# Performance work log

Measured on AMD Instinct MI355X. Metric: run time of the kernel, lower is better.

The kernel has to match this reference:

```python
import jax, jax.numpy as jnp
import numpy as np

H = 12  # num_attention_heads
D = 64  # size_per_head


def setup_inputs() -> dict:
    key = jax.random.key(0)
    ks = jax.random.split(key, 6)
    B, S, W = 4, 2048, H * D
    x = jax.random.normal(ks[0], (B, S, W), dtype=jnp.float32)
    segment_ids = jax.random.randint(ks[1], (B, S), 0, 2, dtype=jnp.int32)
    std = 0.02
    Wq = jax.random.normal(ks[2], (W, W), dtype=jnp.float32) * std
    Wk = jax.random.normal(ks[3], (W, W), dtype=jnp.float32) * std
    Wv = jax.random.normal(ks[4], (W, W), dtype=jnp.float32) * std
    zeros = jnp.zeros((W,), dtype=jnp.float32)
    return {"x": x, "segment_ids": segment_ids, "Wq": Wq, "bq": zeros,
            "Wk": Wk, "bk": zeros, "Wv": Wv, "bv": zeros}


def reference(x, segment_ids, Wq, bq, Wk, bk, Wv, bv):
    B, S, W = x.shape
    # linear projections (no activation; defaults are None)
    q = (x @ Wq + bq).reshape(B, S, H, D).transpose(0, 2, 1, 3)  # [B,H,S,D]
    k = (x @ Wk + bk).reshape(B, S, H, D).transpose(0, 2, 1, 3)
    v = (x @ Wv + bv).reshape(B, S, H, D).transpose(0, 2, 1, 3)
    scores = jnp.einsum('bhqd,bhkd->bhqk', q, k) / jnp.sqrt(jnp.float32(D))
    # UniLM seq2seq bias: position j visible to i iff cumsum(s)[j] <= cumsum(s)[i]
    idxs = jnp.cumsum(segment_ids.astype(jnp.float32), axis=1)  # [B,S]
    mask = (idxs[:, None, :] <= idxs[:, :, None]).astype(jnp.float32)  # [B,S,S]
    bias = -(1.0 - mask) * 1e12
    scores = scores + bias[:, None, :, :]
    probs = jax.nn.softmax(scores, axis=-1)
    ctx = jnp.einsum('bhqk,bhkd->bhqd', probs, v)  # [B,H,S,D]
    return ctx.transpose(0, 2, 1, 3).reshape(B, S, H * D)
```

## Files before the change

### kernel.cpp

```cpp
#include <hip/hip_runtime.h>
#include <hip/hip_bf16.h>

#define NB 4
#define NS 2048
#define NH 12
#define ND 64
#define NW 768
#define HBUF (NB * NH * NS * ND)
#define QBLK 128
#define QSCALE 0.18033688f

typedef __attribute__((ext_vector_type(8))) short bf16x8;
typedef __attribute__((ext_vector_type(4))) float f32x4;
typedef __attribute__((ext_vector_type(16))) float f32x16;

__device__ inline unsigned short f2bf_bits(float f) {
  __hip_bfloat16 h = __float2bfloat16(f);
  union { __hip_bfloat16 h; unsigned short u; } c; c.h = h; return c.u;
}
__device__ inline void gload16(const void* g, void* l) {
  __builtin_amdgcn_global_load_lds(
      (const __attribute__((address_space(1))) unsigned int*)g,
      (__attribute__((address_space(3))) unsigned int*)l, 16, 0, 0);
}
#define EXP_SC 8388608.0f
#define EXP_BI 1064986882.0f

__global__ __launch_bounds__(256) void prep_kernel(
    const float* __restrict__ x, const int* __restrict__ seg,
    const float* __restrict__ Wq, const float* __restrict__ Wk,
    const float* __restrict__ Wv, __hip_bfloat16* __restrict__ xbf,
    __hip_bfloat16* __restrict__ Wt, int* __restrict__ cum) {
  __shared__ float tile[64][65];
  __shared__ int sums[256];
  const int bid = blockIdx.x;
  const int t = threadIdx.x;

  if (bid < 1024) {
    const int n8 = NB * NS * NW / 8;
    for (int i = bid * 256 + t; i < n8; i += 1024 * 256) {
      const float4 a = ((const float4*)x)[i * 2];
      const float4 b = ((const float4*)x)[i * 2 + 1];
      bf16x8 o;
      o[0] = (short)f2bf_bits(a.x); o[1] = (short)f2bf_bits(a.y);
      o[2] = (short)f2bf_bits(a.z); o[3] = (short)f2bf_bits(a.w);
      o[4] = (short)f2bf_bits(b.x); o[5] = (short)f2bf_bits(b.y);
      o[6] = (short)f2bf_bits(b.z); o[7] = (short)f2bf_bits(b.w);
      *(bf16x8*)((unsigned short*)xbf + (size_t)i * 8) = o;
    }
  } else if (bid < 1456) {
    const int idx = bid - 1024;
    const int m = idx / 144, rem = idx % 144;
    const float* W = (m == 0) ? Wq : ((m == 1) ? Wk : Wv);
    const int rt = (rem / 12) * 64, ct = (rem % 12) * 64;
#pragma unroll
    for (int j = 0; j < 4; ++j) {
      const int r = j * 16 + (t >> 4);
      const int c = (t & 15) * 4;
      const float4 v = *(const float4*)(W + (size_t)(rt + r) * NW + ct + c);
      tile[r][c] = v.x; tile[r][c + 1] = v.y; tile[r][c + 2] = v.z; tile[r][c + 3] = v.w;
    }
    __syncthreads();
#pragma unroll
    for (int j = 0; j < 2; ++j) {
      const int i2 = j * 256 + t;
      const int nn = i2 >> 3, kq = (i2 & 7) * 8;
      bf16x8 o;
#pragma unroll
      for (int e = 0; e < 8; ++e) o[e] = (short)f2bf_bits(tile[kq + e][nn]);
      *(bf16x8*)((unsigned short*)Wt + (size_t)(m * NW + ct + nn) * NW + rt + kq) = o;
    }
  } else {
    const int b = bid - 1456;
    int vals[8];
    int s = 0;
    const int base = b * NS + t * 8;
#pragma unroll
    for (int j = 0; j < 8; ++j) { vals[j] = seg[base + j]; s += vals[j]; }
    sums[t] = s;
    __syncthreads();
    int acc = s;
    for (int off = 1; off < 256; off <<= 1) {
      const int u = (t >= off) ? sums[t - off] : 0;
      __syncthreads();
      acc += u;
      sums[t] = acc;
      __syncthreads();
    }
    int prefix = acc - s;
#pragma unroll
    for (int j = 0; j < 8; ++j) { prefix += vals[j]; cum[base + j] = prefix; }
  }
}

__global__ __launch_bounds__(256) void qkv_gemm_kernel(
    const __hip_bfloat16* __restrict__ A, const __hip_bfloat16* __restrict__ Bt,
    const float* __restrict__ bq, const float* __restrict__ bk,
    const float* __restrict__ bv, __hip_bfloat16* __restrict__ O,
    __hip_bfloat16* __restrict__ Vt) {
  __shared__ __align__(16) char As[128 * 128];
  __shared__ __align__(16) char Bs[128 * 128];
  const int t = threadIdx.x, lane = t & 63, w = t >> 6;
  const int l15 = lane & 15, lhi = lane >> 4;
  const int wg = (blockIdx.x & 7) * 144 + (blockIdx.x >> 3);
  const int r0 = (wg / 18) * 128;
  const int by = wg % 18;
  const int m = by / 6;
  const int c0in = (by % 6) * 128;
  const int wm = w >> 1, wn = w & 1;

  int srow[4], scol[4];
#pragma unroll
  for (int i = 0; i < 4; ++i) {
    const int c = (w * 4 + i) * 64 + lane;
    srow[i] = c >> 3;
    scol[i] = ((c & 7) ^ ((c >> 3) & 7)) * 8;
  }

  const unsigned short* Ag = (const unsigned short*)A + (size_t)r0 * NW;
  const unsigned short* Bg = (const unsigned short*)Bt + (size_t)(m * NW + c0in) * NW;

  f32x4 acc[4][4] = {};
  for (int k0 = 0; k0 < NW; k0 += 64) {
    __syncthreads();
#pragma unroll
    for (int i = 0; i < 4; ++i) {
      gload16(Ag + (size_t)srow[i] * NW + k0 + scol[i], As + (w * 4 + i) * 1024);
      gload16(Bg + (size_t)srow[i] * NW + k0 + scol[i], Bs + (w * 4 + i) * 1024);
    }
    __syncthreads();

    bf16x8 af[4][2], bfr[4][2];
#pragma unroll
    for (int mi = 0; mi < 4; ++mi) {
      const int row = wm * 64 + mi * 16 + l15;
      const char* base = As + row * 128;
      const int sw = (row & 7) << 4;
      af[mi][0] = *(const bf16x8*)(base + ((lhi * 16) ^ sw));
      af[mi][1] = *(const bf16x8*)(base + ((64 + lhi * 16) ^ sw));
    }
#pragma unroll
    for (int ni = 0; ni < 4; ++ni) {
      const int row = wn * 64 + ni * 16 + l15;
      const char* base = Bs + row * 128;
      const int sw = (row & 7) << 4;
      bfr[ni][0] = *(const bf16x8*)(base + ((lhi * 16) ^ sw));
      bfr[ni][1] = *(const bf16x8*)(base + ((64 + lhi * 16) ^ sw));
    }
#pragma unroll
    for (int mi = 0; mi < 4; ++mi)
#pragma unroll
      for (int ni = 0; ni < 4; ++ni) {
        acc[mi][ni] = __builtin_amdgcn_mfma_f32_16x16x32_bf16(af[mi][0], bfr[ni][0], acc[mi][ni], 0, 0, 0);
        acc[mi][ni] = __builtin_amdgcn_mfma_f32_16x16x32_bf16(af[mi][1], bfr[ni][1], acc[mi][ni], 0, 0, 0);
      }
  }

  const int hcol = c0in + wn * 64;
  const int h = hcol >> 6;
  const float* bias = (m == 0) ? bq : ((m == 1) ? bk : bv);
  const float qsc = (m == 0) ? QSCALE : 1.0f;
  float bias4[4];
#pragma unroll
  for (int ni = 0; ni < 4; ++ni) bias4[ni] = bias[hcol + ni * 16 + l15];

  if (m == 2) {
#pragma unroll
    for (int mi = 0; mi < 4; ++mi) {
      const int row0 = r0 + wm * 64 + mi * 16 + lhi * 4;
      const int bb = row0 >> 11, ss = row0 & (NS - 1);
#pragma unroll
      for (int ni = 0; ni < 4; ++ni) {
        const int d = ni * 16 + l15;
        ushort4 pk;
        pk.x = f2bf_bits(acc[mi][ni][0] + bias4[ni]);
        pk.y = f2bf_bits(acc[mi][ni][1] + bias4[ni]);
        pk.z = f2bf_bits(acc[mi][ni][2] + bias4[ni]);
        pk.w = f2bf_bits(acc[mi][ni][3] + bias4[ni]);
        *(ushort4*)((unsigned short*)Vt +
                    (((size_t)bb * NH + h) * ND + d) * NS + ss) = pk;
      }
    }
  } else {
    __hip_bfloat16* Om = O + (size_t)m * HBUF;
#pragma unroll
    for (int mi = 0; mi < 4; ++mi) {
#pragma unroll
      for (int rr = 0; rr < 4; ++rr) {
        const int row = r0 + wm * 64 + mi * 16 + lhi * 4 + rr;
        const int bb = row >> 11, ss = row & (NS - 1);
        __hip_bfloat16* op = Om + (((size_t)bb * NH + h) * NS + ss) * ND;
#pragma unroll
        for (int ni = 0; ni < 4; ++ni)
          op[ni * 16 + l15] = __float2bfloat16((acc[mi][ni][rr] + bias4[ni]) * qsc);
      }
    }
  }
}

__global__ __launch_bounds__(256, 3) void attn_mfma_kernel(
    const __hip_bfloat16* __restrict__ Qg, const __hip_bfloat16* __restrict__ Kg,
    const __hip_bfloat16* __restrict__ Vtg, const int* __restrict__ cum,
    float* __restrict__ out) {
  const int t = threadIdx.x, lane = t & 63, w = t >> 6;
  const int l31 = lane & 31, h = lane >> 5;
  const int id = blockIdx.x;
  const int bh = id % (NB * NH);
  const int qraw = id / (NB * NH);
  int qi = qraw >> 1;
  if (qraw & 1) qi = (NS / QBLK - 1) - qi;
  const int s0 = qi * QBLK;
  const int b = bh / NH;
  const size_t hoff = (size_t)bh * NS * ND;

  __shared__ __align__(16) char KB[3][8192];
  __shared__ __align__(16) char VB[3][8192];
  __shared__ unsigned short cumS[NS];

  {
    const int4* cp = (const int4*)(cum + b * NS);
    const int4 a = cp[t * 2], d4 = cp[t * 2 + 1];
    unsigned short tmp[8];
    tmp[0] = (unsigned short)a.x;  tmp[1] = (unsigned short)a.y;
    tmp[2] = (unsigned short)a.z;  tmp[3] = (unsigned short)a.w;
    tmp[4] = (unsigned short)d4.x; tmp[5] = (unsigned short)d4.y;
    tmp[6] = (unsigned short)d4.z; tmp[7] = (unsigned short)d4.w;
    *(uint4*)(cumS + t * 8) = *(const uint4*)tmp;
  }

  bf16x8 qf[4];
  {
    const unsigned short* qp = (const unsigned short*)Qg + hoff +
                               (size_t)(s0 + w * 32 + l31) * ND + h * 8;
#pragma unroll
    for (int c = 0; c < 4; ++c) qf[c] = *(const bf16x8*)(qp + c * 16);
  }

  __syncthreads();

  const int cqm = cumS[s0 + w * 32 + l31];
  const int qminw = cumS[s0 + w * 32];
  const int cqmax = cumS[s0 + QBLK - 1];

  int nt = 1;
  while (nt < NS / 64 && (int)cumS[nt * 64] <= cqmax) ++nt;

  int koff[2][4], voff[2][4];
#pragma unroll
  for (int nn = 0; nn < 2; ++nn) {
    const int frow = nn * 32 + ((l31 >> 4) << 4) + (((l31 >> 2) & 1) << 3) +
                     (((l31 >> 3) & 1) << 2) + (l31 & 3);
    const int sw = (frow & 7) << 4;
#pragma unroll
    for (int c = 0; c < 4; ++c)
      koff[nn][c] = frow * 128 + ((c * 32 + h * 16) ^ sw);
  }
#pragma unroll
  for (int nd = 0; nd < 2; ++nd) {
    const int vrow = nd * 32 + l31;
    const int sw = (vrow & 7) << 4;
#pragma unroll
    for (int jj = 0; jj < 4; ++jj)
      voff[nd][jj] = vrow * 128 + ((jj * 32 + h * 16) ^ sw);
  }

  int srw[2], sce[2];
#pragma unroll
  for (int i = 0; i < 2; ++i) {
    const int c = (w * 2 + i) * 64 + lane;
    srw[i] = c >> 3;
    sce[i] = ((c & 7) ^ ((c >> 3) & 7)) * 8;
  }
  const unsigned short* KgH = (const unsigned short*)Kg + hoff;
  const unsigned short* VgH = (const unsigned short*)Vtg + hoff;

#define STAGE(kt, Kp, Vp)                                                    \
  {                                                                          \
    const int kk0 = (kt) * 64;                                               \
    _Pragma("unroll")                                                        \
    for (int i = 0; i < 2; ++i) {                                            \
      gload16(KgH + (size_t)(kk0 + srw[i]) * ND + sce[i], (Kp) + (w * 2 + i) * 1024); \
      gload16(VgH + (size_t)srw[i] * NS + kk0 + sce[i], (Vp) + (w * 2 + i) * 1024);   \
    }                                                                        \
  }

  char *Kc = KB[0], *Vc = VB[0];
  char *Kn = KB[1], *Vn = VB[1];
  char *Kf = KB[2], *Vf = VB[2];

  STAGE(0, Kc, Vc);
  STAGE(1, Kn, Vn);

  f32x16 acc_o[2] = {};
  f32x16 acc_l = {};
  const bf16x8 onesA = {(short)0x3F80, (short)0x3F80, (short)0x3F80, (short)0x3F80,
                        (short)0x3F80, (short)0x3F80, (short)0x3F80, (short)0x3F80};

  for (int kt = 0; kt < nt; ++kt) {
    if (kt + 2 < nt) {
      STAGE(kt + 2, Kf, Vf);
      asm volatile("s_waitcnt vmcnt(8)" ::: "memory");
    } else if (kt + 2 == nt) {
      asm volatile("s_waitcnt vmcnt(4)" ::: "memory");
    } else {
      asm volatile("s_waitcnt vmcnt(0)" ::: "memory");
    }
    __builtin_amdgcn_s_barrier();

    const int k0 = kt * 64;

    f32x16 accs[2] = {};
    __builtin_amdgcn_s_setprio(1);
#pragma unroll
    for (int nn = 0; nn < 2; ++nn)
#pragma unroll
      for (int c = 0; c < 4; ++c) {
        const bf16x8 kf = *(const bf16x8*)(Kc + koff[nn][c]);
        accs[nn] = __builtin_amdgcn_mfma_f32_32x32x16_bf16(kf, qf[c], accs[nn], 0, 0, 0);
      }
    __builtin_amdgcn_s_setprio(0);

    const bool bdry = (int)cumS[k0 + 63] > qminw;
    bf16x8 pv[4];
    unsigned* pvu = (unsigned*)pv;
#pragma unroll
    for (int nn = 0; nn < 2; ++nn) {
      if (bdry) {
        const unsigned short* ckp = &cumS[k0 + nn * 32 + h * 8];
        ushort4 cv[4];
        cv[0] = *(const ushort4*)(ckp);
        cv[1] = *(const ushort4*)(ckp + 4);
        cv[2] = *(const ushort4*)(ckp + 16);
        cv[3] = *(const ushort4*)(ckp + 20);
        const unsigned short cks[16] = {cv[0].x, cv[0].y, cv[0].z, cv[0].w,
                                        cv[1].x, cv[1].y, cv[1].z, cv[1].w,
                                        cv[2].x, cv[2].y, cv[2].z, cv[2].w,
                                        cv[3].x, cv[3].y, cv[3].z, cv[3].w};
#pragma unroll
        for (int r = 0; r < 16; r += 2) {
          int i0 = (int)fmaf(accs[nn][r], EXP_SC, EXP_BI);
          int i1 = (int)fmaf(accs[nn][r + 1], EXP_SC, EXP_BI);
          i0 = ((int)cks[r] <= cqm) ? i0 : 0;
          i1 = ((int)cks[r + 1] <= cqm) ? i1 : 0;
          pvu[(nn * 2 + (r >> 3)) * 4 + ((r & 7) >> 1)] =
              __builtin_amdgcn_perm((unsigned)i1, (unsigned)i0, 0x07060302u);
        }
      } else {
#pragma unroll
        for (int r = 0; r < 16; r += 2) {
          const int i0 = (int)fmaf(accs[nn][r], EXP_SC, EXP_BI);
          const int i1 = (int)fmaf(accs[nn][r + 1], EXP_SC, EXP_BI);
          pvu[(nn * 2 + (r >> 3)) * 4 + ((r & 7) >> 1)] =
              __builtin_amdgcn_perm((unsigned)i1, (unsigned)i0, 0x07060302u);
        }
      }
    }

    __builtin_amdgcn_s_setprio(1);
#pragma unroll
    for (int nd = 0; nd < 2; ++nd)
#pragma unroll
      for (int jj = 0; jj < 4; ++jj) {
        const bf16x8 vf = *(const bf16x8*)(Vc + voff[nd][jj]);
        acc_o[nd] = __builtin_amdgcn_mfma_f32_32x32x16_bf16(vf, pv[jj], acc_o[nd], 0, 0, 0);
      }
#pragma unroll
    for (int jj = 0; jj < 4; ++jj)
      acc_l = __builtin_amdgcn_mfma_f32_32x32x16_bf16(onesA, pv[jj], acc_l, 0, 0, 0);
    __builtin_amdgcn_s_setprio(0);

    __builtin_amdgcn_s_barrier();

    char* tk = Kc; Kc = Kn; Kn = Kf; Kf = tk;
    char* tv = Vc; Vc = Vn; Vn = Vf; Vf = tv;
  }

  const float inv = 1.0f / acc_l[0];
  const int qrow = s0 + w * 32 + l31;
  float* op = out + (size_t)(b * NS + qrow) * NW + (bh % NH) * ND;
#pragma unroll
  for (int nd = 0; nd < 2; ++nd)
#pragma unroll
    for (int g = 0; g < 4; ++g) {
      float4 o4;
      o4.x = acc_o[nd][g * 4 + 0] * inv;
      o4.y = acc_o[nd][g * 4 + 1] * inv;
      o4.z = acc_o[nd][g * 4 + 2] * inv;
      o4.w = acc_o[nd][g * 4 + 3] * inv;
      *(float4*)(op + nd * 32 + g * 8 + h * 4) = o4;
    }
}

extern "C" void kernel_launch(void* const* d_in, const int* in_sizes, int n_in,
                              void* d_out, int out_size, void* d_ws, size_t ws_size,
                              hipStream_t stream) {
  (void)in_sizes; (void)n_in; (void)out_size; (void)ws_size;
  const float* x  = (const float*)d_in[0];
  const int* seg  = (const int*)d_in[1];
  const float* Wq = (const float*)d_in[2];
  const float* bq = (const float*)d_in[3];
  const float* Wk = (const float*)d_in[4];
  const float* bk = (const float*)d_in[5];
  const float* Wv = (const float*)d_in[6];
  const float* bv = (const float*)d_in[7];
  float* out = (float*)d_out;

  char* ws = (char*)d_ws;
  int* cum = (int*)ws;
  __hip_bfloat16* QKV = (__hip_bfloat16*)(ws + 32768);
  __hip_bfloat16* Qb = QKV;
  __hip_bfloat16* Kb = QKV + (size_t)HBUF;
  __hip_bfloat16* xbf = QKV + (size_t)3 * HBUF;
  __hip_bfloat16* Wt = xbf + (size_t)HBUF;
  __hip_bfloat16* Vt = Wt + (size_t)3 * NW * NW;

  prep_kernel<<<dim3(1460), dim3(256), 0, stream>>>(x, seg, Wq, Wk, Wv, xbf, Wt, cum);
  qkv_gemm_kernel<<<dim3(1152), dim3(256), 0, stream>>>(xbf, Wt, bq, bk, bv, QKV, Vt);
  attn_mfma_kernel<<<dim3(NS / QBLK * NB * NH), dim3(256), 0, stream>>>(Qb, Kb, Vt, cum, out);
}
```

Measured before the change: 106.3 us.

## Double-buffer QKV GEMM LDS tiles to overlap global loads with MFMA

The QKV projection GEMM now keeps two LDS buffers for the A and B tiles. It issues global-to-LDS loads for the next k-tile before computing the current one, and uses vmcnt waits plus raw barriers in place of two __syncthreads per iteration. It also raises wave priority around the MFMA block. This aims to hide global load latency behind matrix math. The cost is doubled LDS use (64KB), which may reduce occupancy, and correctness now depends on the hand-written waitcnt counts.

```diff
diff --git a/kernel.cpp b/kernel.cpp
--- a/kernel.cpp
+++ b/kernel.cpp
@@ -98,8 +98,8 @@
     const float* __restrict__ bq, const float* __restrict__ bk,
     const float* __restrict__ bv, __hip_bfloat16* __restrict__ O,
     __hip_bfloat16* __restrict__ Vt) {
-  __shared__ __align__(16) char As[128 * 128];
-  __shared__ __align__(16) char Bs[128 * 128];
+  __shared__ __align__(16) char AB[2][16384];
+  __shared__ __align__(16) char BB[2][16384];
   const int t = threadIdx.x, lane = t & 63, w = t >> 6;
   const int l15 = lane & 15, lhi = lane >> 4;
   const int wg = (blockIdx.x & 7) * 144 + (blockIdx.x >> 3);
@@ -120,21 +120,35 @@
   const unsigned short* Ag = (const unsigned short*)A + (size_t)r0 * NW;
   const unsigned short* Bg = (const unsigned short*)Bt + (size_t)(m * NW + c0in) * NW;
 
+#define QSTAGE(k0v, Ap, Bp)                                                   \
+  {                                                                           \
+    _Pragma("unroll")                                                         \
+    for (int i = 0; i < 4; ++i) {                                             \
+      gload16(Ag + (size_t)srow[i] * NW + (k0v) + scol[i], (Ap) + (w * 4 + i) * 1024); \
+      gload16(Bg + (size_t)srow[i] * NW + (k0v) + scol[i], (Bp) + (w * 4 + i) * 1024); \
+    }                                                                         \
+  }
+
+  QSTAGE(0, AB[0], BB[0]);
+
   f32x4 acc[4][4] = {};
-  for (int k0 = 0; k0 < NW; k0 += 64) {
-    __syncthreads();
-#pragma unroll
-    for (int i = 0; i < 4; ++i) {
-      gload16(Ag + (size_t)srow[i] * NW + k0 + scol[i], As + (w * 4 + i) * 1024);
-      gload16(Bg + (size_t)srow[i] * NW + k0 + scol[i], Bs + (w * 4 + i) * 1024);
-    }
-    __syncthreads();
-
+  const int NT = NW / 64;
+  for (int kt = 0; kt < NT; ++kt) {
+    if (kt + 1 < NT) {
+      QSTAGE((kt + 1) * 64, AB[(kt + 1) & 1], BB[(kt + 1) & 1]);
+      asm volatile("s_waitcnt vmcnt(8)" ::: "memory");
+    } else {
+      asm volatile("s_waitcnt vmcnt(0)" ::: "memory");
+    }
+    __builtin_amdgcn_s_barrier();
+
+    const char* Ac = AB[kt & 1];
+    const char* Bc = BB[kt & 1];
     bf16x8 af[4][2], bfr[4][2];
 #pragma unroll
     for (int mi = 0; mi < 4; ++mi) {
       const int row = wm * 64 + mi * 16 + l15;
-      const char* base = As + row * 128;
+      const char* base = Ac + row * 128;
       const int sw = (row & 7) << 4;
       af[mi][0] = *(const bf16x8*)(base + ((lhi * 16) ^ sw));
       af[mi][1] = *(const bf16x8*)(base + ((64 + lhi * 16) ^ sw));
@@ -142,11 +156,12 @@
 #pragma unroll
     for (int ni = 0; ni < 4; ++ni) {
       const int row = wn * 64 + ni * 16 + l15;
-      const char* base = Bs + row * 128;
+      const char* base = Bc + row * 128;
       const int sw = (row & 7) << 4;
       bfr[ni][0] = *(const bf16x8*)(base + ((lhi * 16) ^ sw));
       bfr[ni][1] = *(const bf16x8*)(base + ((64 + lhi * 16) ^ sw));
     }
+    __builtin_amdgcn_s_setprio(1);
 #pragma unroll
     for (int mi = 0; mi < 4; ++mi)
 #pragma unroll
@@ -154,6 +169,9 @@
         acc[mi][ni] = __builtin_amdgcn_mfma_f32_16x16x32_bf16(af[mi][0], bfr[ni][0], acc[mi][ni], 0, 0, 0);
         acc[mi][ni] = __builtin_amdgcn_mfma_f32_16x16x32_bf16(af[mi][1], bfr[ni][1], acc[mi][ni], 0, 0, 0);
       }
+    __builtin_amdgcn_s_setprio(0);
+
+    __builtin_amdgcn_s_barrier();
   }
 
   const int hcol = c0in + wn * 64;
```

After: 100.8 us (median of 2 runs). 1.06x faster.
